# Performance work log

Measured on AMD Instinct MI355X. Metric: run time of the kernel, lower is better.

## Reference

```python
import jax, jax.numpy as jnp
import numpy as np

# Tap offsets (dy, dx) within the 3x3 footprint for each kernel_type.
# kernel_type 0 -> 5-tap skeleton (center + 4-neighbors), 1 -> full 3x3, else -> 3-tap row.
TAPS = {
    0: [(1, 1), (0, 1), (1, 0), (1, 2), (2, 1)],
    1: [(i, j) for i in range(3) for j in range(3)],
    2: [(1, 0), (1, 1), (1, 2)],
}

KERNEL_TYPE = 0
STRIDE = 1
PAD = 1
DIL = 1
SPATIAL = False


def setup_inputs() -> dict:
    key = jax.random.key(0)
    k1, k2 = jax.random.split(key)
    N, Ci, H, W = 16, 256, 64, 64
    Co, K = 256, len(TAPS[KERNEL_TYPE])
    x = jax.random.normal(k1, (N, Ci, H, W), dtype=jnp.float32)
    # kaiming-uniform-ish scale
    bound = np.sqrt(6.0 / (Ci * K))
    weight = jax.random.uniform(k2, (Co, Ci, K), dtype=jnp.float32, minval=-bound, maxval=bound)
    return {"x": x, "weight": weight, "step": 0}


def _spatial_conv(x, weight):
    # x: [N, Ci, H, W], weight: [Co, Ci, K]
    taps = TAPS[KERNEL_TYPE]
    N, Ci, H, W = x.shape
    Hout = (H + 2 * PAD - (DIL * 2 + 1)) // STRIDE + 1
    Wout = (W + 2 * PAD - (DIL * 2 + 1)) // STRIDE + 1
    xp = jnp.pad(x, ((0, 0), (0, 0), (PAD, PAD), (PAD, PAD)))
    outs = []
    for k, (dy, dx) in enumerate(taps):
        y0, x0 = dy * DIL, dx * DIL
        xs = xp[:, :, y0:y0 + (Hout - 1) * STRIDE + 1:STRIDE,
                      x0:x0 + (Wout - 1) * STRIDE + 1:STRIDE]  # [N, Ci, Hout, Wout]
        outs.append(jnp.einsum('nchw,oc->nohw', xs, weight[:, :, k]))
    return jnp.stack(outs, axis=0)  # [K, N, Co, Hout, Wout]


def reference(x, weight, step):
    out = _spatial_conv(x, weight)  # [K, N, Co, H, W]
    if SPATIAL:
        K, N, Co, Ho, Wo = out.shape
        out = jnp.transpose(out, (1, 0, 2, 3, 4)).reshape(N, K * Co, Ho, Wo)
    else:
        out = out.sum(axis=0)  # sum over taps -> [N, Co, H, W]
    return out
```

## Files before the change

kernel.cpp:

```cpp
#include <hip/hip_runtime.h>
#include <hip/hip_bf16.h>
#include <cstddef>

#define N_  16
#define CI  256
#define CO  256
#define KT  5

#define XBUF_B   25344
#define WOFF     50688
#define WBUF_B   40960
#define SMEM_B   132608

typedef __attribute__((ext_vector_type(8)))  short  short8;
typedef __attribute__((ext_vector_type(8)))  unsigned short ushort8;
typedef __attribute__((ext_vector_type(4)))  unsigned int uint4v;
typedef __attribute__((ext_vector_type(16))) float  floatx16;

static __device__ __forceinline__ unsigned short f2bf(float f) {
    union { float f; unsigned u; } v; v.f = f;
    unsigned r = v.u + 0x7fff + ((v.u >> 16) & 1);
    return (unsigned short)(r >> 16);
}

typedef const __attribute__((address_space(1))) unsigned int g_u32;
typedef __attribute__((address_space(3))) unsigned int l_u32;
static __device__ __forceinline__ void gload_lds16(const void* g, void* l) {
    __builtin_amdgcn_global_load_lds((g_u32*)g, (l_u32*)l, 16, 0, 0);
}

__global__ void wtrans_kernel(const float* __restrict__ w, unsigned short* __restrict__ wb) {
    int idx = blockIdx.x * 256 + threadIdx.x;
    if (idx >= KT * CO * CI) return;
    int e  = idx & 7;
    int o  = (idx >> 3) & 255;
    int lh = (idx >> 11) & 1;
    int ks = (idx >> 12) & 1;
    int c  = (idx >> 13) & 7;
    int k  = idx >> 16;
    int ci = c * 32 + ks * 16 + lh * 8 + e;
    wb[idx] = f2bf(w[(size_t)o * (CI * KT) + ci * KT + k]);
}

template<int KS>
static __device__ __forceinline__ void compute_half(const char* wB, const char* xB,
                                                    floatx16 (&acc)[2][2][2]) {
    #pragma unroll
    for (int k = 0; k < KT; ++k) {
        const int dy = (k == 1) ? 0 : (k == 4) ? 2 : 1;
        const int dx = (k == 2) ? 0 : (k == 3) ? 2 : 1;
        const short8 a0 = *(const short8*)(wB + k * 8192);
        const short8 a1 = *(const short8*)(wB + k * 8192 + 512);
        #pragma unroll
        for (int hr = 0; hr < 2; ++hr) {
            #pragma unroll
            for (int wh = 0; wh < 2; ++wh) {
                const short8 b = *(const short8*)(xB +
                    ((hr + dy) * 264 + KS * 132 + wh * 32 + dx) * 16);
                acc[0][hr][wh] = __builtin_amdgcn_mfma_f32_32x32x16_bf16(a0, b, acc[0][hr][wh], 0, 0, 0);
                acc[1][hr][wh] = __builtin_amdgcn_mfma_f32_32x32x16_bf16(a1, b, acc[1][hr][wh], 0, 0, 0);
            }
        }
    }
}

__global__ __launch_bounds__(512, 2) void conv_mfma(const float* __restrict__ x,
                                                    const unsigned short* __restrict__ wb,
                                                    float* __restrict__ out) {
    extern __shared__ char smem[];

    const int tid = threadIdx.x;
    const int bx0 = blockIdx.x;
    const int bx  = (bx0 & 7) * 32 + (bx0 >> 3);
    const int hq  = bx & 15;
    const int n   = bx >> 4;
    const int h0  = hq * 4;

    const int lane    = tid & 63;
    const int wv      = tid >> 6;
    const int l31     = lane & 31;
    const int lh      = lane >> 5;
    const int owave   = (wv & 3) * 64;
    const int rowbase = (wv >> 2) * 2;

    const int sw  = tid & 63;
    const int scg = (tid >> 6) & 3;
    const int sr3 = tid >> 8;

    if (tid < 96) {
        int buf = tid & 1;
        int wp  = ((tid >> 1) & 1) * 65;
        int cg  = (tid >> 2) & 3;
        int r   = tid >> 4;
        ((ushort8*)smem)[buf * 1584 + r * 264 + cg * 66 + wp] = (ushort8)0;
    }

    const float* xn = x + (size_t)n * CI * 4096;

    float zm[3];
    int   hcl[3];
    #pragma unroll
    for (int ii = 0; ii < 3; ++ii) {
        int hh = h0 - 1 + sr3 * 3 + ii;
        zm[ii]  = ((unsigned)hh < 64u) ? 1.f : 0.f;
        hcl[ii] = hh < 0 ? 0 : (hh > 63 ? 63 : hh);
    }

    float xr[3][8];
    auto load_chunk = [&](int c) {
        #pragma unroll
        for (int ii = 0; ii < 3; ++ii) {
            const float* p = xn + (c * 32 + scg * 8) * 4096 + hcl[ii] * 64 + sw;
            #pragma unroll
            for (int e = 0; e < 8; ++e) xr[ii][e] = p[e * 4096];
        }
    };
    auto write_chunk = [&](int b) {
        #pragma unroll
        for (int ii = 0; ii < 3; ++ii) {
            const int i = sr3 * 3 + ii;
            uint4v v;
            #pragma unroll
            for (int e = 0; e < 4; ++e) {
                __hip_bfloat162 pk = __float22bfloat162_rn(
                    make_float2(zm[ii] * xr[ii][2 * e], zm[ii] * xr[ii][2 * e + 1]));
                union { __hip_bfloat162 h; unsigned u; } cv; cv.h = pk;
                v[e] = cv.u;
            }
            *(uint4v*)&((ushort8*)smem)[b * 1584 + i * 264 + scg * 66 + (sw + 1)] = v;
        }
    };
    auto stage_w = [&](int c, int ks, int buf) {
        const char* src = (const char*)wb + c * 16384 + ks * 8192 + wv * 1024 + lane * 16;
        char* dst = smem + WOFF + buf * WBUF_B + wv * 1024;
        #pragma unroll
        for (int i = 0; i < 5; ++i)
            gload_lds16(src + (size_t)i * 131072, dst + i * 8192);
    };

    floatx16 acc[2][2][2];
    #pragma unroll
    for (int ot = 0; ot < 2; ++ot)
        #pragma unroll
        for (int hr = 0; hr < 2; ++hr)
            #pragma unroll
            for (int wh = 0; wh < 2; ++wh)
                #pragma unroll
                for (int e = 0; e < 16; ++e) acc[ot][hr][wh][e] = 0.f;

    const char* xbase = smem + rowbase * 4224 + lh * 1056 + l31 * 16;
    const char* wbase = smem + WOFF + lh * 4096 + (owave + l31) * 16;

    stage_w(0, 0, 0);
    load_chunk(0);
    write_chunk(0);
    __builtin_amdgcn_sched_barrier(0);
    asm volatile("s_waitcnt vmcnt(0) lgkmcnt(0)" ::: "memory");
    __builtin_amdgcn_s_barrier();
    __builtin_amdgcn_sched_barrier(0);

    for (int c = 0; c < 8; ++c) {
        const char* xb = xbase + (c & 1) * XBUF_B;

        stage_w(c, 1, 1);
        asm volatile("" ::: "memory");
        if (c < 7) load_chunk(c + 1);
        asm volatile("" ::: "memory");
        compute_half<0>(wbase, xb, acc);
        __builtin_amdgcn_sched_barrier(0);
        if (c < 7) asm volatile("s_waitcnt vmcnt(24) lgkmcnt(0)" ::: "memory");
        else       asm volatile("s_waitcnt vmcnt(0) lgkmcnt(0)"  ::: "memory");
        __builtin_amdgcn_s_barrier();
        __builtin_amdgcn_sched_barrier(0);

        if (c < 7) stage_w(c + 1, 0, 0);
        asm volatile("" ::: "memory");
        if (c < 7) write_chunk((c + 1) & 1);
        asm volatile("" ::: "memory");
        compute_half<1>(wbase + WBUF_B, xb, acc);
        __builtin_amdgcn_sched_barrier(0);
        if (c < 7) {
            asm volatile("s_waitcnt vmcnt(0) lgkmcnt(0)" ::: "memory");
            __builtin_amdgcn_s_barrier();
            __builtin_amdgcn_sched_barrier(0);
        }
    }

    #pragma unroll
    for (int ot = 0; ot < 2; ++ot) {
        #pragma unroll
        for (int hr = 0; hr < 2; ++hr) {
            const int h = h0 + rowbase + hr;
            #pragma unroll
            for (int wh = 0; wh < 2; ++wh) {
                #pragma unroll
                for (int reg = 0; reg < 16; ++reg) {
                    int o = owave + ot * 32 + (reg & 3) + 8 * (reg >> 2) + 4 * lh;
                    out[(((size_t)n * CO + o) * 64 + h) * 64 + wh * 32 + l31] = acc[ot][hr][wh][reg];
                }
            }
        }
    }
}

extern "C" void kernel_launch(void* const* d_in, const int* in_sizes, int n_in,
                              void* d_out, int out_size, void* d_ws, size_t ws_size,
                              hipStream_t stream) {
    const float* x = (const float*)d_in[0];
    const float* w = (const float*)d_in[1];
    float* out = (float*)d_out;

    unsigned short* wb = (unsigned short*)d_ws;

    static bool attr_set = false;
    if (!attr_set) {
        hipFuncSetAttribute(reinterpret_cast<const void*>(conv_mfma),
                            hipFuncAttributeMaxDynamicSharedMemorySize, SMEM_B);
        attr_set = true;
    }

    wtrans_kernel<<<dim3((KT * CO * CI + 255) / 256), dim3(256), 0, stream>>>(w, wb);
    conv_mfma<<<dim3(N_ * 16), dim3(512), SMEM_B, stream>>>(x, wb, out);
}
```

Measured before the change: 137.0 us.

## Load weight fragments directly from global into registers instead of LDS staging

Removes the async global-to-LDS staging of bf16 weights and has each wave read its MFMA A-operand fragments straight from global memory into registers before each half-chunk. LDS then holds only the double-buffered input tile, shrinking shared memory from ~130KB to ~50KB, and the hand-tuned waitcnt/barrier pipeline becomes simpler __syncthreads. The cost is that global weight loads now sit directly before the MFMAs and can stall them, and the second half's weight loads are not overlapped with compute.

Measured after the change: 143.0 us. 4.4% more time.

```diff
diff --git a/kernel.cpp b/kernel.cpp
--- a/kernel.cpp
+++ b/kernel.cpp
@@ -7,10 +7,8 @@
 #define CO  256
 #define KT  5
 
-#define XBUF_B   25344
-#define WOFF     50688
-#define WBUF_B   40960
-#define SMEM_B   132608
+#define XCELLS  1584
+#define XBUF_B  25344
 
 typedef __attribute__((ext_vector_type(8)))  short  short8;
 typedef __attribute__((ext_vector_type(8)))  unsigned short ushort8;
@@ -21,12 +19,6 @@
     union { float f; unsigned u; } v; v.f = f;
     unsigned r = v.u + 0x7fff + ((v.u >> 16) & 1);
     return (unsigned short)(r >> 16);
-}
-
-typedef const __attribute__((address_space(1))) unsigned int g_u32;
-typedef __attribute__((address_space(3))) unsigned int l_u32;
-static __device__ __forceinline__ void gload_lds16(const void* g, void* l) {
-    __builtin_amdgcn_global_load_lds((g_u32*)g, (l_u32*)l, 16, 0, 0);
 }
 
 __global__ void wtrans_kernel(const float* __restrict__ w, unsigned short* __restrict__ wb) {
@@ -43,22 +35,20 @@
 }
 
 template<int KS>
-static __device__ __forceinline__ void compute_half(const char* wB, const char* xB,
+static __device__ __forceinline__ void compute_half(const short8 (&a)[KT][2], const char* xB,
                                                     floatx16 (&acc)[2][2][2]) {
     #pragma unroll
     for (int k = 0; k < KT; ++k) {
         const int dy = (k == 1) ? 0 : (k == 4) ? 2 : 1;
         const int dx = (k == 2) ? 0 : (k == 3) ? 2 : 1;
-        const short8 a0 = *(const short8*)(wB + k * 8192);
-        const short8 a1 = *(const short8*)(wB + k * 8192 + 512);
         #pragma unroll
         for (int hr = 0; hr < 2; ++hr) {
             #pragma unroll
             for (int wh = 0; wh < 2; ++wh) {
                 const short8 b = *(const short8*)(xB +
                     ((hr + dy) * 264 + KS * 132 + wh * 32 + dx) * 16);
-                acc[0][hr][wh] = __builtin_amdgcn_mfma_f32_32x32x16_bf16(a0, b, acc[0][hr][wh], 0, 0, 0);
-                acc[1][hr][wh] = __builtin_amdgcn_mfma_f32_32x32x16_bf16(a1, b, acc[1][hr][wh], 0, 0, 0);
+                acc[0][hr][wh] = __builtin_amdgcn_mfma_f32_32x32x16_bf16(a[k][0], b, acc[0][hr][wh], 0, 0, 0);
+                acc[1][hr][wh] = __builtin_amdgcn_mfma_f32_32x32x16_bf16(a[k][1], b, acc[1][hr][wh], 0, 0, 0);
             }
         }
     }
@@ -67,7 +57,7 @@
 __global__ __launch_bounds__(512, 2) void conv_mfma(const float* __restrict__ x,
                                                     const unsigned short* __restrict__ wb,
                                                     float* __restrict__ out) {
-    extern __shared__ char smem[];
+    __shared__ ushort8 lds[2 * XCELLS];
 
     const int tid = threadIdx.x;
     const int bx0 = blockIdx.x;
@@ -92,7 +82,7 @@
         int wp  = ((tid >> 1) & 1) * 65;
         int cg  = (tid >> 2) & 3;
         int r   = tid >> 4;
-        ((ushort8*)smem)[buf * 1584 + r * 264 + cg * 66 + wp] = (ushort8)0;
+        lds[buf * XCELLS + r * 264 + cg * 66 + wp] = (ushort8)0;
     }
 
     const float* xn = x + (size_t)n * CI * 4096;
@@ -127,15 +117,8 @@
                 union { __hip_bfloat162 h; unsigned u; } cv; cv.h = pk;
                 v[e] = cv.u;
             }
-            *(uint4v*)&((ushort8*)smem)[b * 1584 + i * 264 + scg * 66 + (sw + 1)] = v;
+            *(uint4v*)&lds[b * XCELLS + i * 264 + scg * 66 + (sw + 1)] = v;
         }
-    };
-    auto stage_w = [&](int c, int ks, int buf) {
-        const char* src = (const char*)wb + c * 16384 + ks * 8192 + wv * 1024 + lane * 16;
-        char* dst = smem + WOFF + buf * WBUF_B + wv * 1024;
-        #pragma unroll
-        for (int i = 0; i < 5; ++i)
-            gload_lds16(src + (size_t)i * 131072, dst + i * 8192);
     };
 
     floatx16 acc[2][2][2];
@@ -148,42 +131,41 @@
                 #pragma unroll
                 for (int e = 0; e < 16; ++e) acc[ot][hr][wh][e] = 0.f;
 
-    const char* xbase = smem + rowbase * 4224 + lh * 1056 + l31 * 16;
-    const char* wbase = smem + WOFF + lh * 4096 + (owave + l31) * 16;
+    const char* xbase = (const char*)lds + rowbase * 4224 + lh * 1056 + l31 * 16;
+    const unsigned short* wA = wb + lh * 2048 + (owave + l31) * 8;
 
-    stage_w(0, 0, 0);
     load_chunk(0);
     write_chunk(0);
-    __builtin_amdgcn_sched_barrier(0);
-    asm volatile("s_waitcnt vmcnt(0) lgkmcnt(0)" ::: "memory");
-    __builtin_amdgcn_s_barrier();
-    __builtin_amdgcn_sched_barrier(0);
+    __syncthreads();
 
     for (int c = 0; c < 8; ++c) {
         const char* xb = xbase + (c & 1) * XBUF_B;
+        const unsigned short* wc = wA + c * 8192;
 
-        stage_w(c, 1, 1);
-        asm volatile("" ::: "memory");
-        if (c < 7) load_chunk(c + 1);
-        asm volatile("" ::: "memory");
-        compute_half<0>(wbase, xb, acc);
-        __builtin_amdgcn_sched_barrier(0);
-        if (c < 7) asm volatile("s_waitcnt vmcnt(24) lgkmcnt(0)" ::: "memory");
-        else       asm volatile("s_waitcnt vmcnt(0) lgkmcnt(0)"  ::: "memory");
-        __builtin_amdgcn_s_barrier();
+        short8 a[KT][2];
+        #pragma unroll
+        for (int k = 0; k < KT; ++k)
+            #pragma unroll
+            for (int ot = 0; ot < 2; ++ot)
+                a[k][ot] = *(const short8*)(wc + k * 65536 + ot * 256);
         __builtin_amdgcn_sched_barrier(0);
 
-        if (c < 7) stage_w(c + 1, 0, 0);
-        asm volatile("" ::: "memory");
+        if (c < 7) load_chunk(c + 1);
+        __builtin_amdgcn_sched_barrier(0);
+
+        compute_half<0>(a, xb, acc);
+        __builtin_amdgcn_sched_barrier(0);
+
+        #pragma unroll
+        for (int k = 0; k < KT; ++k)
+            #pragma unroll
+            for (int ot = 0; ot < 2; ++ot)
+                a[k][ot] = *(const short8*)(wc + k * 65536 + 4096 + ot * 256);
+        compute_half<1>(a, xb, acc);
+        __builtin_amdgcn_sched_barrier(0);
+
         if (c < 7) write_chunk((c + 1) & 1);
-        asm volatile("" ::: "memory");
-        compute_half<1>(wbase + WBUF_B, xb, acc);
-        __builtin_amdgcn_sched_barrier(0);
-        if (c < 7) {
-            asm volatile("s_waitcnt vmcnt(0) lgkmcnt(0)" ::: "memory");
-            __builtin_amdgcn_s_barrier();
-            __builtin_amdgcn_sched_barrier(0);
-        }
+        __syncthreads();
     }
 
     #pragma unroll
@@ -212,13 +194,6 @@
 
     unsigned short* wb = (unsigned short*)d_ws;
 
-    static bool attr_set = false;
-    if (!attr_set) {
-        hipFuncSetAttribute(reinterpret_cast<const void*>(conv_mfma),
-                            hipFuncAttributeMaxDynamicSharedMemorySize, SMEM_B);
-        attr_set = true;
-    }
-
     wtrans_kernel<<<dim3((KT * CO * CI + 255) / 256), dim3(256), 0, stream>>>(w, wb);
-    conv_mfma<<<dim3(N_ * 16), dim3(512), SMEM_B, stream>>>(x, wb, out);
+    conv_mfma<<<dim3(N_ * 16), dim3(512), 0, stream>>>(x, wb, out);
 }
```
